# Performance work log

Hardware: AMD Instinct MI355X
Metric: run time of the kernel (lower is better)

The kernel has to match this reference:

```python
import jax, jax.numpy as jnp
import numpy as np

D = 2048          # n_embd
H = 4 * D         # hidden_size
B, S = 4, 2048


def _make_masks(seed=0):
    rng = np.random.default_rng(seed)
    # mask1: for each group of 4 output rows, keep 2 of 4 rows (whole rows)
    mask1 = np.zeros((H, D), dtype=np.float32)
    for i in range(0, H, 4):
        keep = rng.permutation(4)[:2] + i
        mask1[keep, :] = 1.0
    # mask2: for each group of 4 input columns, keep 2 of 4 columns
    mask2 = np.zeros((D, H), dtype=np.float32)
    for i in range(0, H, 4):
        keep = rng.permutation(4)[:2] + i
        mask2[:, keep] = 1.0
    return jnp.asarray(mask1), jnp.asarray(mask2)


def setup_inputs() -> dict:
    key = jax.random.key(0)
    k_x, k_w1, k_w2 = jax.random.split(key, 3)
    x = jax.random.normal(k_x, (B, S, D), dtype=jnp.float32)
    # Kaiming-uniform-ish init like nn.Linear defaults
    w1 = jax.random.uniform(k_w1, (H, D), dtype=jnp.float32, minval=-1.0, maxval=1.0) / np.sqrt(D)
    w2 = jax.random.uniform(k_w2, (D, H), dtype=jnp.float32, minval=-1.0, maxval=1.0) / np.sqrt(H)
    mask1, mask2 = _make_masks()
    return {"x": x, "w1": w1, "w2": w2, "mask1": mask1, "mask2": mask2}


def reference(x, w1, w2, mask1, mask2):
    # sparse_multiply is elementwise mask application on the weights
    sw1 = w1 * mask1                      # [H, D]
    sw2 = w2 * mask2                      # [D, H]
    h = jnp.einsum('bsd,hd->bsh', x, sw1) # F.linear(x, sw1)
    h = jax.nn.gelu(h, approximate=False) # torch F.gelu default = exact erf
    out = jnp.einsum('bsh,dh->bsd', h, sw2)
    return out
```

## Files before the change

kernel.cpp:

```cpp
#include <hip/hip_runtime.h>
#include <hip/hip_bf16.h>

typedef __bf16 bf16_t;
typedef __bf16 bf16x8 __attribute__((ext_vector_type(8)));
typedef float f32x4 __attribute__((ext_vector_type(4)));

__device__ __forceinline__ unsigned short f32_to_bf16_rn(float f) {
  unsigned u = __float_as_uint(f);
  u += 0x7fffu + ((u >> 16) & 1u);
  return (unsigned short)(u >> 16);
}

__device__ __forceinline__ ushort4 cvt4(float4 v) {
  ushort4 o;
  o.x = f32_to_bf16_rn(v.x);
  o.y = f32_to_bf16_rn(v.y);
  o.z = f32_to_bf16_rn(v.z);
  o.w = f32_to_bf16_rn(v.w);
  return o;
}

__device__ __forceinline__ float gelu_exact(float x) {
  return 0.5f * x * (1.0f + erff(x * 0.7071067811865475f));
}

#define GLDS16(g, l)                                                          \
  __builtin_amdgcn_global_load_lds(                                           \
      (const __attribute__((address_space(1))) void*)(g),                     \
      (__attribute__((address_space(3))) void*)(l), 16, 0, 0)

__global__ void build_idx_kernel(const float* __restrict__ mask1,
                                 const float* __restrict__ mask2,
                                 int* __restrict__ idx, int* __restrict__ meta,
                                 int H, int D) {
  __shared__ int sums[1024];
  const int t = threadIdx.x;
  int flags[8];
  int tot = 0;
#pragma unroll
  for (int u = 0; u < 8; ++u) {
    int j = t * 8 + u;
    int f = (mask1[(long long)j * D] != 0.0f) && (mask2[j] != 0.0f);
    flags[u] = f;
    tot += f;
  }
  sums[t] = tot;
  __syncthreads();
  for (int off = 1; off < 1024; off <<= 1) {
    int v = (t >= off) ? sums[t - off] : 0;
    __syncthreads();
    sums[t] += v;
    __syncthreads();
  }
  int pos = sums[t] - tot;
#pragma unroll
  for (int u = 0; u < 8; ++u) {
    if (flags[u]) idx[pos++] = t * 8 + u;
  }
  if (t == 1023) {
    int count = sums[1023];
    meta[0] = count;
    meta[1] = (count + 127) & ~127;
  }
}

__global__ void prep_kernel(const float* __restrict__ x,
                            const float* __restrict__ w1,
                            const int* __restrict__ idx,
                            const int* __restrict__ meta,
                            unsigned short* __restrict__ xb,
                            unsigned short* __restrict__ w1c, int D) {
  const int nx = 4194304;
  const int count = meta[0];
  const int kpad = meta[1];
  const int nw1 = kpad << 9;
  for (int i = blockIdx.x * 256 + threadIdx.x; i < nx + nw1; i += 2048 * 256) {
    if (i < nx) {
      ((ushort4*)xb)[i] = cvt4(((const float4*)x)[i]);
    } else {
      int q = i - nx;
      int k = q >> 9;
      int d4 = (q & 511) << 2;
      ushort4 o = {0, 0, 0, 0};
      if (k < count)
        o = cvt4(*(const float4*)(w1 + (long long)idx[k] * D + d4));
      *(ushort4*)(w1c + (long long)k * D + d4) = o;
    }
  }
}

#define POOLG 2048
#define W2BLKS 512

template <int EPI, int DOW2>
__global__ __launch_bounds__(256, 4) void gemm_pool_kernel(
    const bf16_t* __restrict__ A, const bf16_t* __restrict__ B,
    void* __restrict__ Cout, long long ldA, long long ldB, long long ldC,
    int Kfix, int ncolFix, const int* __restrict__ meta,
    const float* __restrict__ w2src, const int* __restrict__ idx,
    unsigned short* __restrict__ w2c, int H) {
  if (DOW2 && blockIdx.x >= POOLG) {
    const int nq = 2097152;
    const int count = meta[0];
    for (int q = (blockIdx.x - POOLG) * 256 + threadIdx.x; q < nq;
         q += W2BLKS * 256) {
      int n = q >> 10;
      int k4 = (q & 1023) << 2;
      ushort4 o = {0, 0, 0, 0};
      const float* src = w2src + (long long)n * H;
#pragma unroll
      for (int u = 0; u < 4; ++u) {
        int k = k4 + u;
        unsigned short v = 0;
        if (k < count) v = f32_to_bf16_rn(src[idx[k]]);
        ((unsigned short*)&o)[u] = v;
      }
      *(ushort4*)(w2c + (long long)n * 4096 + k4) = o;
    }
    return;
  }

  const int kpad = meta[1];
  const int K = (EPI == 0) ? kpad : Kfix;
  const int ncol = (EPI == 1) ? (kpad >> 7) : ncolFix;
  const int ntiles = ncol << 6;
  const int NT = K >> 6;
  const int phase = ((blockIdx.x >> 8) & 3) * (NT >> 2);

  __shared__ bf16_t As[128 * 64];
  __shared__ bf16_t Bs[128 * 64];

  const int tid = threadIdx.x;
  const int l = tid & 63;
  const int w = tid >> 6;
  const int wm = w >> 1;
  const int wn = w & 1;

  const int srow = tid >> 3;
  const int sg = ((tid & 7) ^ ((tid >> 3) & 7)) * 8;

  const int fr = l & 15;
  const int gA = (l >> 4) ^ (l & 7);

  for (int tau = blockIdx.x; tau < ntiles; tau += POOLG) {
    const int row = tau & 63;
    const int col = tau >> 6;
    const long long brow = (long long)row * 128;
    const long long bcol = (long long)col * 128;

    const bf16_t* Ag = A + (brow + srow) * ldA + sg;
    const bf16_t* Bg = B + (bcol + srow) * ldB + sg;

    f32x4 acc[4][4];
#pragma unroll
    for (int m = 0; m < 4; ++m)
#pragma unroll
      for (int n = 0; n < 4; ++n) acc[m][n] = (f32x4){0.f, 0.f, 0.f, 0.f};

    for (int it = 0; it < NT; ++it) {
      int t = it + phase;
      if (t >= NT) t -= NT;
      const int k0 = t << 6;
      GLDS16(Ag + k0, &As[tid * 8]);
      GLDS16(Ag + 32 * ldA + k0, &As[2048 + tid * 8]);
      GLDS16(Ag + 64 * ldA + k0, &As[4096 + tid * 8]);
      GLDS16(Ag + 96 * ldA + k0, &As[6144 + tid * 8]);
      GLDS16(Bg + k0, &Bs[tid * 8]);
      GLDS16(Bg + 32 * ldB + k0, &Bs[2048 + tid * 8]);
      GLDS16(Bg + 64 * ldB + k0, &Bs[4096 + tid * 8]);
      GLDS16(Bg + 96 * ldB + k0, &Bs[6144 + tid * 8]);
      __syncthreads();
#pragma unroll
      for (int kk = 0; kk < 2; ++kk) {
        const int gp = (gA ^ (kk * 4)) * 8;
        bf16x8 af[4], bfr[4];
#pragma unroll
        for (int m = 0; m < 4; ++m)
          af[m] = *(const bf16x8*)(&As[(wm * 64 + m * 16 + fr) * 64 + gp]);
#pragma unroll
        for (int n = 0; n < 4; ++n)
          bfr[n] = *(const bf16x8*)(&Bs[(wn * 64 + n * 16 + fr) * 64 + gp]);
#pragma unroll
        for (int m = 0; m < 4; ++m)
#pragma unroll
          for (int n = 0; n < 4; ++n)
            acc[m][n] = __builtin_amdgcn_mfma_f32_16x16x32_bf16(
                af[m], bfr[n], acc[m][n], 0, 0, 0);
      }
      __syncthreads();
    }

    const int orow = wm * 64 + (l >> 4) * 4;
    const int ocol = wn * 64 + fr;
#pragma unroll
    for (int m = 0; m < 4; ++m)
#pragma unroll
      for (int n = 0; n < 4; ++n)
#pragma unroll
        for (int r = 0; r < 4; ++r) {
          long long rr = brow + orow + m * 16 + r;
          long long cc = bcol + ocol + n * 16;
          float v = acc[m][n][r];
          if (EPI == 1) {
            ((unsigned short*)Cout)[rr * ldC + cc] =
                f32_to_bf16_rn(gelu_exact(v));
          } else {
            ((float*)Cout)[rr * ldC + cc] = v;
          }
        }
  }
}

extern "C" void kernel_launch(void* const* d_in, const int* in_sizes, int n_in,
                              void* d_out, int out_size, void* d_ws,
                              size_t ws_size, hipStream_t stream) {
  const float* x = (const float*)d_in[0];
  const float* w1 = (const float*)d_in[1];
  const float* w2 = (const float*)d_in[2];
  const float* mask1 = (const float*)d_in[3];
  const float* mask2 = (const float*)d_in[4];
  float* out = (float*)d_out;

  const int D = 2048, H = 8192, M = 8192;
  const int KP = 4096;

  char* ws = (char*)d_ws;
  unsigned short* xb = (unsigned short*)ws;
  unsigned short* w1c = xb + (size_t)M * D;
  unsigned short* w2c = w1c + (size_t)KP * D;
  unsigned short* hb = w2c + (size_t)D * KP;
  int* idx = (int*)(hb + (size_t)M * KP);
  int* meta = idx + KP;

  build_idx_kernel<<<1, 1024, 0, stream>>>(mask1, mask2, idx, meta, H, D);

  prep_kernel<<<2048, 256, 0, stream>>>(x, w1, idx, meta, xb, w1c, D);

  gemm_pool_kernel<1, 1><<<POOLG + W2BLKS, 256, 0, stream>>>(
      (const bf16_t*)xb, (const bf16_t*)w1c, hb, (long long)D, (long long)D,
      (long long)KP, D, 0, meta, w2, idx, w2c, H);

  gemm_pool_kernel<0, 0><<<1024, 256, 0, stream>>>(
      (const bf16_t*)hb, (const bf16_t*)w2c, out, (long long)KP,
      (long long)KP, (long long)D, 0, 16, meta, nullptr, nullptr, nullptr, H);
}
```

Before: 239.6 us.

## Move w2 gather into prep kernel and shrink first GEMM grid

The w2 column gather/convert, which used to run in extra blocks appended to the first GEMM launch, now runs as a third segment of the prep kernel. The first GEMM launches with 1024 blocks instead of 2048 plus 512, and its tile loop strides by gridDim.x. This drops the co-scheduled gather that competed with GEMM blocks for CUs and bandwidth, at the cost of serializing the gather before GEMM1. The GEMM1 tile-to-block mapping also changes, so each block now handles multiple tiles.

```diff
diff --git a/kernel.cpp b/kernel.cpp
--- a/kernel.cpp
+++ b/kernel.cpp
@@ -66,18 +66,22 @@
 
 __global__ void prep_kernel(const float* __restrict__ x,
                             const float* __restrict__ w1,
+                            const float* __restrict__ w2,
                             const int* __restrict__ idx,
                             const int* __restrict__ meta,
                             unsigned short* __restrict__ xb,
-                            unsigned short* __restrict__ w1c, int D) {
+                            unsigned short* __restrict__ w1c,
+                            unsigned short* __restrict__ w2c, int D, int H) {
   const int nx = 4194304;
   const int count = meta[0];
   const int kpad = meta[1];
   const int nw1 = kpad << 9;
-  for (int i = blockIdx.x * 256 + threadIdx.x; i < nx + nw1; i += 2048 * 256) {
+  const int nw2 = 2097152;
+  const int total = nx + nw1 + nw2;
+  for (int i = blockIdx.x * 256 + threadIdx.x; i < total; i += 2048 * 256) {
     if (i < nx) {
       ((ushort4*)xb)[i] = cvt4(((const float4*)x)[i]);
-    } else {
+    } else if (i < nx + nw1) {
       int q = i - nx;
       int k = q >> 9;
       int d4 = (q & 511) << 2;
@@ -85,29 +89,12 @@
       if (k < count)
         o = cvt4(*(const float4*)(w1 + (long long)idx[k] * D + d4));
       *(ushort4*)(w1c + (long long)k * D + d4) = o;
-    }
-  }
-}
-
-#define POOLG 2048
-#define W2BLKS 512
-
-template <int EPI, int DOW2>
-__global__ __launch_bounds__(256, 4) void gemm_pool_kernel(
-    const bf16_t* __restrict__ A, const bf16_t* __restrict__ B,
-    void* __restrict__ Cout, long long ldA, long long ldB, long long ldC,
-    int Kfix, int ncolFix, const int* __restrict__ meta,
-    const float* __restrict__ w2src, const int* __restrict__ idx,
-    unsigned short* __restrict__ w2c, int H) {
-  if (DOW2 && blockIdx.x >= POOLG) {
-    const int nq = 2097152;
-    const int count = meta[0];
-    for (int q = (blockIdx.x - POOLG) * 256 + threadIdx.x; q < nq;
-         q += W2BLKS * 256) {
+    } else {
+      int q = i - nx - nw1;
       int n = q >> 10;
       int k4 = (q & 1023) << 2;
       ushort4 o = {0, 0, 0, 0};
-      const float* src = w2src + (long long)n * H;
+      const float* src = w2 + (long long)n * H;
 #pragma unroll
       for (int u = 0; u < 4; ++u) {
         int k = k4 + u;
@@ -117,9 +104,14 @@
       }
       *(ushort4*)(w2c + (long long)n * 4096 + k4) = o;
     }
-    return;
-  }
-
+  }
+}
+
+template <int EPI>
+__global__ __launch_bounds__(256, 4) void gemm_pool_kernel(
+    const bf16_t* __restrict__ A, const bf16_t* __restrict__ B,
+    void* __restrict__ Cout, long long ldA, long long ldB, long long ldC,
+    int Kfix, int ncolFix, const int* __restrict__ meta) {
   const int kpad = meta[1];
   const int K = (EPI == 0) ? kpad : Kfix;
   const int ncol = (EPI == 1) ? (kpad >> 7) : ncolFix;
@@ -142,7 +134,7 @@
   const int fr = l & 15;
   const int gA = (l >> 4) ^ (l & 7);
 
-  for (int tau = blockIdx.x; tau < ntiles; tau += POOLG) {
+  for (int tau = blockIdx.x; tau < ntiles; tau += gridDim.x) {
     const int row = tau & 63;
     const int col = tau >> 6;
     const long long brow = (long long)row * 128;
@@ -234,13 +226,14 @@
 
   build_idx_kernel<<<1, 1024, 0, stream>>>(mask1, mask2, idx, meta, H, D);
 
-  prep_kernel<<<2048, 256, 0, stream>>>(x, w1, idx, meta, xb, w1c, D);
-
-  gemm_pool_kernel<1, 1><<<POOLG + W2BLKS, 256, 0, stream>>>(
+  prep_kernel<<<2048, 256, 0, stream>>>(x, w1, w2, idx, meta, xb, w1c, w2c, D,
+                                        H);
+
+  gemm_pool_kernel<1><<<1024, 256, 0, stream>>>(
       (const bf16_t*)xb, (const bf16_t*)w1c, hb, (long long)D, (long long)D,
-      (long long)KP, D, 0, meta, w2, idx, w2c, H);
-
-  gemm_pool_kernel<0, 0><<<1024, 256, 0, stream>>>(
+      (long long)KP, D, 0, meta);
+
+  gemm_pool_kernel<0><<<1024, 256, 0, stream>>>(
       (const bf16_t*)hb, (const bf16_t*)w2c, out, (long long)KP,
-      (long long)KP, (long long)D, 0, 16, meta, nullptr, nullptr, nullptr, H);
-}
+      (long long)KP, (long long)D, 0, 16, meta);
+}
```

New measurement: 240.7 us (median of 2 runs). About the same (+0.4%).
